# Optimization experiments

Hardware: AMD Instinct MI355X
Metric: run time of the kernel (lower is better)

The kernel has to match this reference:

```python
import jax, jax.numpy as jnp
import numpy as np

HIDDEN = 2048
NUM_Q_HEADS = 32
NUM_KV_HEADS = 8
HEAD_DIM = HIDDEN // NUM_Q_HEADS  # 64
GROUPS = NUM_Q_HEADS // NUM_KV_HEADS  # 4
MAX_WAVELENGTH = 10000.0
B, S = 2, 1024
NEG_INF = -1e9  # keras Softmax masking constant


def apply_rope(x, start_index=0, max_wavelength=MAX_WAVELENGTH):
    # x: [b, s, h, d]; keras_hub RotaryEmbedding (split-half / Llama style)
    d = x.shape[-1]
    s = x.shape[1]
    freq_range = jnp.arange(0, d, 2, dtype=jnp.float32)
    inverse_freq = 1.0 / (max_wavelength ** (freq_range / d))  # [d/2]
    positions = jnp.arange(s, dtype=jnp.float32) + start_index
    freq = positions[:, None] * inverse_freq[None, :]  # [s, d/2]
    emb = jnp.concatenate([freq, freq], axis=-1)[None, :, None, :]  # [1,s,1,d]
    cos = jnp.cos(emb).astype(x.dtype)
    sin = jnp.sin(emb).astype(x.dtype)
    x1, x2 = jnp.split(x, 2, axis=-1)
    half_rot = jnp.concatenate([-x2, x1], axis=-1)
    return x * cos + half_rot * sin


def setup_inputs() -> dict:
    key = jax.random.key(0)
    k1, k2, k3, k4, k5 = jax.random.split(key, 5)
    hidden_states = jax.random.normal(k1, (B, S, HIDDEN), dtype=jnp.float32)
    # causal mask, broadcast over batch
    attention_mask = jnp.broadcast_to(
        jnp.tril(jnp.ones((S, S), dtype=bool))[None], (B, S, S)
    )
    scale = 1.0 / np.sqrt(HIDDEN)
    Wq = jax.random.normal(k2, (HIDDEN, NUM_Q_HEADS * HEAD_DIM), dtype=jnp.float32) * scale
    Wk = jax.random.normal(k3, (HIDDEN, NUM_KV_HEADS * HEAD_DIM), dtype=jnp.float32) * scale
    Wv = jax.random.normal(k4, (HIDDEN, NUM_KV_HEADS * HEAD_DIM), dtype=jnp.float32) * scale
    Wo = jax.random.normal(k5, (NUM_Q_HEADS * HEAD_DIM, HIDDEN), dtype=jnp.float32) * scale
    return {"hidden_states": hidden_states, "attention_mask": attention_mask,
            "Wq": Wq, "Wk": Wk, "Wv": Wv, "Wo": Wo}


def reference(hidden_states, attention_mask, Wq, Wk, Wv, Wo):
    b, s, _ = hidden_states.shape
    q = (hidden_states @ Wq).reshape(b, s, NUM_Q_HEADS, HEAD_DIM)
    k = (hidden_states @ Wk).reshape(b, s, NUM_KV_HEADS, HEAD_DIM)
    v = (hidden_states @ Wv).reshape(b, s, NUM_KV_HEADS, HEAD_DIM)
    q = apply_rope(q)
    k = apply_rope(k)
    # GQA: repeat kv heads to match query heads (ops.repeat on axis 2)
    k = jnp.repeat(k, GROUPS, axis=2)
    v = jnp.repeat(v, GROUPS, axis=2)
    inv_norm = 1.0 / np.sqrt(HEAD_DIM)
    scores = jnp.einsum("bquh,bkuh->buqk", q, k) * inv_norm  # [b, h, q, k]
    scores = scores.astype(jnp.float32)
    scores = jnp.where(attention_mask[:, None, :, :], scores, NEG_INF)
    probs = jax.nn.softmax(scores, axis=-1).astype(hidden_states.dtype)
    attn = jnp.einsum("buqk,bkuh->bquh", probs, v)  # [b, q, h, hd]
    attn = attn.reshape(b, s, HIDDEN)
    return attn @ Wo
```

## Files before the change

kernel.cpp:

```cpp
#include <hip/hip_runtime.h>
#include <hip/hip_bf16.h>
#include <math.h>

#define S_LEN 1024
#define BATCH 2
#define HIDDEN 2048
#define NQH 32
#define NKVH 8
#define HD 64
#define LDQKV 3072
#define M_ROWS (BATCH * S_LEN)

typedef __attribute__((ext_vector_type(8))) short bf16x8;
typedef __attribute__((ext_vector_type(4))) float f32x4;

typedef unsigned int uint32_g __attribute__((address_space(1)));
typedef unsigned int uint32_l __attribute__((address_space(3)));

static __device__ __forceinline__ void load_lds16(const void* g, void* l) {
    __builtin_amdgcn_global_load_lds((const uint32_g*)g, (uint32_l*)l, 16, 0, 0);
}

static __device__ __forceinline__ short f2bf(float f) {
    union { __hip_bfloat16 h; short s; } cv;
    cv.h = __float2bfloat16(f);
    return cv.s;
}

__global__ __launch_bounds__(256) void conv_all_kernel(
    const float* __restrict__ X,
    const float* __restrict__ Wq, const float* __restrict__ Wk,
    const float* __restrict__ Wv, const float* __restrict__ Wo,
    short* __restrict__ Xb, short* __restrict__ Wqkvt, short* __restrict__ Wot,
    float2* __restrict__ cs2)
{
    __shared__ short Ts[64][68];
    const int tid = threadIdx.x;

    if (blockIdx.z == 4) {
        int flat = blockIdx.y * 32 + blockIdx.x;
        size_t base = (size_t)flat * 4096 + (size_t)tid * 16;
        #pragma unroll
        for (int rep = 0; rep < 2; ++rep) {
            size_t i = base + rep * 8;
            float4 a = *reinterpret_cast<const float4*>(X + i);
            float4 b = *reinterpret_cast<const float4*>(X + i + 4);
            union { bf16x8 v; short s[8]; } t;
            t.s[0] = f2bf(a.x); t.s[1] = f2bf(a.y); t.s[2] = f2bf(a.z); t.s[3] = f2bf(a.w);
            t.s[4] = f2bf(b.x); t.s[5] = f2bf(b.y); t.s[6] = f2bf(b.z); t.s[7] = f2bf(b.w);
            *reinterpret_cast<bf16x8*>(Xb + i) = t.v;
        }
        if (flat < 128) {
            int g = flat * 256 + tid;
            int s = g >> 5, i = g & 31;
            float inv_freq = 1.0f / powf(10000.0f, (float)i / 32.0f);
            float freq = (float)s * inv_freq;
            double sn, cs;
            sincos((double)freq, &sn, &cs);
            cs2[g] = make_float2((float)cs, (float)sn);
        }
        return;
    }

    const float* src; short* dst; int N;
    switch (blockIdx.z) {
        case 0: src = Wq; dst = Wqkvt;                         N = 2048; break;
        case 1: src = Wk; dst = Wqkvt + (size_t)2048 * 2048;   N = 512;  break;
        case 2: src = Wv; dst = Wqkvt + (size_t)2560 * 2048;   N = 512;  break;
        default: src = Wo; dst = Wot;                          N = 2048; break;
    }
    const int n0 = blockIdx.x * 64, k0 = blockIdx.y * 64;
    if (n0 >= N) return;

    #pragma unroll
    for (int rep = 0; rep < 4; ++rep) {
        int idx = rep * 256 + tid;
        int row = idx >> 4, c4 = (idx & 15) * 4;
        float4 v = *reinterpret_cast<const float4*>(
            src + (size_t)(k0 + row) * N + n0 + c4);
        ushort4 u;
        u.x = (unsigned short)f2bf(v.x); u.y = (unsigned short)f2bf(v.y);
        u.z = (unsigned short)f2bf(v.z); u.w = (unsigned short)f2bf(v.w);
        *reinterpret_cast<ushort4*>(&Ts[row][c4]) = u;
    }
    __syncthreads();
    #pragma unroll
    for (int rep = 0; rep < 2; ++rep) {
        int idx = rep * 256 + tid;
        int n = idx >> 3, kc = (idx & 7) * 8;
        union { bf16x8 v; short s[8]; } t;
        #pragma unroll
        for (int j = 0; j < 8; ++j) t.s[j] = Ts[kc + j][n];
        *reinterpret_cast<bf16x8*>(dst + (size_t)(n0 + n) * 2048 + k0 + kc) = t.v;
    }
}

template <bool ROPE_BF16>
__global__ __launch_bounds__(256) void gemm_bf16_kernel(
    const short* __restrict__ A, const short* __restrict__ Bt,
    float* __restrict__ C, short* __restrict__ Cb,
    const float2* __restrict__ cs2, int K, int ldc)
{
    const int n0 = blockIdx.x * 128, m0 = blockIdx.y * 128;
    const int tid = threadIdx.x;
    const int w = tid >> 6, lane = tid & 63;
    const int wm = w & 1, wn = w >> 1;
    const int m15 = lane & 15, q4 = lane >> 4;

    __shared__ short As[128][64];
    __shared__ short Bs[128][64];

    f32x4 acc[4][4];
    #pragma unroll
    for (int i = 0; i < 4; ++i)
        #pragma unroll
        for (int j = 0; j < 4; ++j) acc[i][j] = (f32x4){0.f, 0.f, 0.f, 0.f};

    const int srow = lane >> 3;
    const int pchunk = lane & 7;

    for (int k0 = 0; k0 < K; k0 += 64) {
        __syncthreads();
        #pragma unroll
        for (int r = 0; r < 4; ++r) {
            int row = (w * 4 + r) * 8 + srow;
            int lchunk = pchunk ^ (row & 7);
            load_lds16(A + (size_t)(m0 + row) * K + k0 + lchunk * 8,
                       &As[(w * 4 + r) * 8][0]);
            load_lds16(Bt + (size_t)(n0 + row) * K + k0 + lchunk * 8,
                       &Bs[(w * 4 + r) * 8][0]);
        }
        __syncthreads();

        #pragma unroll
        for (int ch = 0; ch < 2; ++ch) {
            bf16x8 af[4], bf[4];
            #pragma unroll
            for (int mt = 0; mt < 4; ++mt) {
                int row = wm * 64 + mt * 16 + m15;
                af[mt] = *reinterpret_cast<const bf16x8*>(
                    &As[row][(((ch * 4 + q4) ^ (row & 7))) * 8]);
            }
            #pragma unroll
            for (int nt = 0; nt < 4; ++nt) {
                int row = wn * 64 + nt * 16 + m15;
                bf[nt] = *reinterpret_cast<const bf16x8*>(
                    &Bs[row][(((ch * 4 + q4) ^ (row & 7))) * 8]);
            }
            #pragma unroll
            for (int mt = 0; mt < 4; ++mt)
                #pragma unroll
                for (int nt = 0; nt < 4; ++nt)
                    acc[mt][nt] = __builtin_amdgcn_mfma_f32_16x16x32_bf16(
                        af[mt], bf[nt], acc[mt][nt], 0, 0, 0);
        }
    }

    const int colbase = n0 + wn * 64;
    if (!ROPE_BF16) {
        #pragma unroll
        for (int mt = 0; mt < 4; ++mt)
            #pragma unroll
            for (int nt = 0; nt < 4; ++nt)
                #pragma unroll
                for (int reg = 0; reg < 4; ++reg)
                    C[(size_t)(m0 + wm * 64 + mt * 16 + q4 * 4 + reg) * ldc
                      + colbase + nt * 16 + m15] = acc[mt][nt][reg];
    } else if (colbase >= 2560) {
        #pragma unroll
        for (int mt = 0; mt < 4; ++mt)
            #pragma unroll
            for (int nt = 0; nt < 4; ++nt)
                #pragma unroll
                for (int reg = 0; reg < 4; ++reg)
                    Cb[(size_t)(m0 + wm * 64 + mt * 16 + q4 * 4 + reg) * ldc
                       + colbase + nt * 16 + m15] = f2bf(acc[mt][nt][reg]);
    } else {
        #pragma unroll
        for (int mt = 0; mt < 4; ++mt) {
            #pragma unroll
            for (int reg = 0; reg < 4; ++reg) {
                int row = m0 + wm * 64 + mt * 16 + q4 * 4 + reg;
                int s = row & (S_LEN - 1);
                float2 t0 = cs2[s * 32 + m15];
                float2 t1 = cs2[s * 32 + 16 + m15];
                float a0 = acc[mt][0][reg], a1 = acc[mt][1][reg];
                float a2 = acc[mt][2][reg], a3 = acc[mt][3][reg];
                size_t base = (size_t)row * ldc + colbase + m15;
                Cb[base +  0] = f2bf(a0 * t0.x - a2 * t0.y);
                Cb[base + 16] = f2bf(a1 * t1.x - a3 * t1.y);
                Cb[base + 32] = f2bf(a2 * t0.x + a0 * t0.y);
                Cb[base + 48] = f2bf(a3 * t1.x + a1 * t1.y);
            }
        }
    }
}

__global__ __launch_bounds__(256) void vtrans_kernel(
    const short* __restrict__ qkvb, short* __restrict__ vt_g)
{
    __shared__ short Ts[128][72];
    const int k0 = blockIdx.x * 128;
    const int bk = blockIdx.y;
    const int b = bk >> 3, kvh = bk & 7;
    const int tid = threadIdx.x;

    #pragma unroll
    for (int rep = 0; rep < 4; ++rep) {
        int idx = rep * 256 + tid;
        int key = idx >> 3, c8 = (idx & 7) * 8;
        *reinterpret_cast<bf16x8*>(&Ts[key][c8]) =
            *reinterpret_cast<const bf16x8*>(
                qkvb + (size_t)(b * S_LEN + k0 + key) * LDQKV + 2560 + kvh * 64 + c8);
    }
    __syncthreads();
    #pragma unroll
    for (int rep = 0; rep < 4; ++rep) {
        int idx = rep * 256 + tid;
        int dim = idx >> 4, kc = (idx & 15) * 8;
        union { bf16x8 v; short s[8]; } t;
        #pragma unroll
        for (int j = 0; j < 8; ++j) t.s[j] = Ts[kc + j][dim];
        *reinterpret_cast<bf16x8*>(
            vt_g + (size_t)(bk * 64 + dim) * S_LEN + k0 + kc) = t.v;
    }
}

__global__ __launch_bounds__(512) void attn_kernel(
    const short* __restrict__ qkvb, const short* __restrict__ vt_g,
    short* __restrict__ attn_b)
{
    const int qt = 7 - blockIdx.x;
    const int h  = blockIdx.y;
    const int b  = blockIdx.z;
    const int tid = threadIdx.x;
    const int w = tid >> 6, lane = tid & 63;
    const int kvh = h >> 2;
    const int m15 = lane & 15, q4 = lane >> 4;

    __shared__ short Ks[64][72];
    __shared__ short Vt[64][72];
    __shared__ float Ps[8][16][68];

    const int rowbase = qt * 128 + w * 16;
    const bf16x8 qf0 = *reinterpret_cast<const bf16x8*>(
        qkvb + (size_t)(b * S_LEN + rowbase + m15) * LDQKV + h * HD + q4 * 8);
    const bf16x8 qf1 = *reinterpret_cast<const bf16x8*>(
        qkvb + (size_t)(b * S_LEN + rowbase + m15) * LDQKV + h * HD + 32 + q4 * 8);

    f32x4 o4[4];
    #pragma unroll
    for (int i = 0; i < 4; ++i) o4[i] = (f32x4){0.f, 0.f, 0.f, 0.f};
    float lsum[4] = {0.f, 0.f, 0.f, 0.f};

    const int ntiles = qt * 2 + 2;
    const int j8 = tid >> 3, c8 = (tid & 7) * 8;
    const short* kbase = qkvb + (size_t)(b * S_LEN) * LDQKV + 2048 + kvh * HD;
    const short* vbase = vt_g + (size_t)((b * 8 + kvh) * 64 + j8) * S_LEN;

    for (int t = 0; t < ntiles; ++t) {
        __syncthreads();
        *reinterpret_cast<bf16x8*>(&Ks[j8][c8]) =
            *reinterpret_cast<const bf16x8*>(kbase + (size_t)(t * 64 + j8) * LDQKV + c8);
        *reinterpret_cast<bf16x8*>(&Vt[j8][c8]) =
            *reinterpret_cast<const bf16x8*>(vbase + t * 64 + c8);
        __syncthreads();

        #pragma unroll
        for (int nt = 0; nt < 4; ++nt) {
            f32x4 acc = (f32x4){0.f, 0.f, 0.f, 0.f};
            bf16x8 kf0 = *reinterpret_cast<const bf16x8*>(&Ks[nt * 16 + m15][q4 * 8]);
            bf16x8 kf1 = *reinterpret_cast<const bf16x8*>(&Ks[nt * 16 + m15][32 + q4 * 8]);
            acc = __builtin_amdgcn_mfma_f32_16x16x32_bf16(qf0, kf0, acc, 0, 0, 0);
            acc = __builtin_amdgcn_mfma_f32_16x16x32_bf16(qf1, kf1, acc, 0, 0, 0);
            int colg = t * 64 + nt * 16 + m15;
            #pragma unroll
            for (int reg = 0; reg < 4; ++reg) {
                int rowg = rowbase + q4 * 4 + reg;
                float sc = acc[reg] * 0.125f;
                float p = (colg <= rowg) ? __expf(fminf(sc, 60.f)) : 0.f;
                lsum[reg] += p;
                Ps[w][q4 * 4 + reg][nt * 16 + m15] = p;
            }
        }

        bf16x8 pf[2];
        #pragma unroll
        for (int ch = 0; ch < 2; ++ch) {
            f32x4 pa = *reinterpret_cast<const f32x4*>(&Ps[w][m15][ch * 32 + q4 * 8]);
            f32x4 pb = *reinterpret_cast<const f32x4*>(&Ps[w][m15][ch * 32 + q4 * 8 + 4]);
            union { bf16x8 v; short s[8]; } tb;
            tb.s[0] = f2bf(pa[0]); tb.s[1] = f2bf(pa[1]);
            tb.s[2] = f2bf(pa[2]); tb.s[3] = f2bf(pa[3]);
            tb.s[4] = f2bf(pb[0]); tb.s[5] = f2bf(pb[1]);
            tb.s[6] = f2bf(pb[2]); tb.s[7] = f2bf(pb[3]);
            pf[ch] = tb.v;
        }

        #pragma unroll
        for (int nt2 = 0; nt2 < 4; ++nt2) {
            bf16x8 vf0 = *reinterpret_cast<const bf16x8*>(&Vt[nt2 * 16 + m15][q4 * 8]);
            bf16x8 vf1 = *reinterpret_cast<const bf16x8*>(&Vt[nt2 * 16 + m15][32 + q4 * 8]);
            o4[nt2] = __builtin_amdgcn_mfma_f32_16x16x32_bf16(pf[0], vf0, o4[nt2], 0, 0, 0);
            o4[nt2] = __builtin_amdgcn_mfma_f32_16x16x32_bf16(pf[1], vf1, o4[nt2], 0, 0, 0);
        }
    }

    float invl[4];
    #pragma unroll
    for (int reg = 0; reg < 4; ++reg) {
        float l = lsum[reg];
        l += __shfl_xor(l, 1, 64);
        l += __shfl_xor(l, 2, 64);
        l += __shfl_xor(l, 4, 64);
        l += __shfl_xor(l, 8, 64);
        invl[reg] = 1.0f / l;
    }

    #pragma unroll
    for (int nt2 = 0; nt2 < 4; ++nt2)
        #pragma unroll
        for (int reg = 0; reg < 4; ++reg)
            attn_b[(size_t)(b * S_LEN + rowbase + q4 * 4 + reg) * HIDDEN
                   + h * HD + nt2 * 16 + m15] = f2bf(o4[nt2][reg] * invl[reg]);
}

extern "C" void kernel_launch(void* const* d_in, const int* in_sizes, int n_in,
                              void* d_out, int out_size, void* d_ws, size_t ws_size,
                              hipStream_t stream) {
    const float* X  = (const float*)d_in[0];
    const float* Wq = (const float*)d_in[2];
    const float* Wk = (const float*)d_in[3];
    const float* Wv = (const float*)d_in[4];
    const float* Wo = (const float*)d_in[5];
    float* out = (float*)d_out;

    short*  qkvb  = (short*)d_ws;
    short*  Xb    = qkvb + (size_t)M_ROWS * LDQKV;
    short*  Wqkvt = Xb + (size_t)HIDDEN * HIDDEN;
    short*  Wot   = Wqkvt + (size_t)LDQKV * HIDDEN;
    short*  vt_g  = Wot + (size_t)HIDDEN * HIDDEN;
    float2* cs2   = (float2*)(vt_g + (size_t)16 * 64 * S_LEN);
    short*  attn_b = Xb;

    conv_all_kernel<<<dim3(32, 32, 5), dim3(256), 0, stream>>>(
        X, Wq, Wk, Wv, Wo, Xb, Wqkvt, Wot, cs2);

    gemm_bf16_kernel<true><<<dim3(24, 16), dim3(256), 0, stream>>>(
        Xb, Wqkvt, nullptr, qkvb, cs2, 2048, LDQKV);
    vtrans_kernel<<<dim3(8, 16), dim3(256), 0, stream>>>(qkvb, vt_g);
    attn_kernel<<<dim3(8, 32, 2), dim3(512), 0, stream>>>(qkvb, vt_g, attn_b);
    gemm_bf16_kernel<false><<<dim3(16, 16), dim3(256), 0, stream>>>(
        attn_b, Wot, out, nullptr, nullptr, 2048, HIDDEN);
}
```

Measured before the change: 231.9 us.

## Shrink GEMM tiles to 128x64 and fuse V transpose into QKV GEMM epilogue

The GEMM tile shrinks from 128x128 to 128x64, doubling the grid (768 and 512 blocks) so more of the CUs are busy. The standalone V-transpose kernel is removed. Blocks covering V columns now transpose their bf16 tile through LDS and write vt_g directly, saving one launch and a round trip through global memory. In exchange, each tile gets less reuse of A per K step, and V blocks no longer write V into qkvb (attention reads only vt_g).

```diff
diff --git a/kernel.cpp b/kernel.cpp
--- a/kernel.cpp
+++ b/kernel.cpp
@@ -99,20 +99,21 @@
 __global__ __launch_bounds__(256) void gemm_bf16_kernel(
     const short* __restrict__ A, const short* __restrict__ Bt,
     float* __restrict__ C, short* __restrict__ Cb,
+    short* __restrict__ vt_g,
     const float2* __restrict__ cs2, int K, int ldc)
 {
-    const int n0 = blockIdx.x * 128, m0 = blockIdx.y * 128;
+    const int n0 = blockIdx.x * 64, m0 = blockIdx.y * 128;
     const int tid = threadIdx.x;
     const int w = tid >> 6, lane = tid & 63;
-    const int wm = w & 1, wn = w >> 1;
     const int m15 = lane & 15, q4 = lane >> 4;
 
-    __shared__ short As[128][64];
-    __shared__ short Bs[128][64];
-
-    f32x4 acc[4][4];
-    #pragma unroll
-    for (int i = 0; i < 4; ++i)
+    __shared__ short SL[128 * 64 + 64 * 64];
+    short (*As)[64] = (short(*)[64])SL;
+    short (*Bs)[64] = (short(*)[64])(SL + 128 * 64);
+
+    f32x4 acc[2][4];
+    #pragma unroll
+    for (int i = 0; i < 2; ++i)
         #pragma unroll
         for (int j = 0; j < 4; ++j) acc[i][j] = (f32x4){0.f, 0.f, 0.f, 0.f};
 
@@ -127,28 +128,33 @@
             int lchunk = pchunk ^ (row & 7);
             load_lds16(A + (size_t)(m0 + row) * K + k0 + lchunk * 8,
                        &As[(w * 4 + r) * 8][0]);
+        }
+        #pragma unroll
+        for (int r = 0; r < 2; ++r) {
+            int row = (w * 2 + r) * 8 + srow;
+            int lchunk = pchunk ^ (row & 7);
             load_lds16(Bt + (size_t)(n0 + row) * K + k0 + lchunk * 8,
-                       &Bs[(w * 4 + r) * 8][0]);
+                       &Bs[(w * 2 + r) * 8][0]);
         }
         __syncthreads();
 
         #pragma unroll
         for (int ch = 0; ch < 2; ++ch) {
-            bf16x8 af[4], bf[4];
-            #pragma unroll
-            for (int mt = 0; mt < 4; ++mt) {
-                int row = wm * 64 + mt * 16 + m15;
+            bf16x8 af[2], bf[4];
+            #pragma unroll
+            for (int mt = 0; mt < 2; ++mt) {
+                int row = w * 32 + mt * 16 + m15;
                 af[mt] = *reinterpret_cast<const bf16x8*>(
                     &As[row][(((ch * 4 + q4) ^ (row & 7))) * 8]);
             }
             #pragma unroll
             for (int nt = 0; nt < 4; ++nt) {
-                int row = wn * 64 + nt * 16 + m15;
+                int row = nt * 16 + m15;
                 bf[nt] = *reinterpret_cast<const bf16x8*>(
                     &Bs[row][(((ch * 4 + q4) ^ (row & 7))) * 8]);
             }
             #pragma unroll
-            for (int mt = 0; mt < 4; ++mt)
+            for (int mt = 0; mt < 2; ++mt)
                 #pragma unroll
                 for (int nt = 0; nt < 4; ++nt)
                     acc[mt][nt] = __builtin_amdgcn_mfma_f32_16x16x32_bf16(
@@ -156,73 +162,58 @@
         }
     }
 
-    const int colbase = n0 + wn * 64;
     if (!ROPE_BF16) {
         #pragma unroll
-        for (int mt = 0; mt < 4; ++mt)
+        for (int mt = 0; mt < 2; ++mt)
             #pragma unroll
             for (int nt = 0; nt < 4; ++nt)
                 #pragma unroll
                 for (int reg = 0; reg < 4; ++reg)
-                    C[(size_t)(m0 + wm * 64 + mt * 16 + q4 * 4 + reg) * ldc
-                      + colbase + nt * 16 + m15] = acc[mt][nt][reg];
-    } else if (colbase >= 2560) {
-        #pragma unroll
-        for (int mt = 0; mt < 4; ++mt)
-            #pragma unroll
-            for (int nt = 0; nt < 4; ++nt)
-                #pragma unroll
-                for (int reg = 0; reg < 4; ++reg)
-                    Cb[(size_t)(m0 + wm * 64 + mt * 16 + q4 * 4 + reg) * ldc
-                       + colbase + nt * 16 + m15] = f2bf(acc[mt][nt][reg]);
-    } else {
-        #pragma unroll
-        for (int mt = 0; mt < 4; ++mt) {
+                    C[(size_t)(m0 + w * 32 + mt * 16 + q4 * 4 + reg) * ldc
+                      + n0 + nt * 16 + m15] = acc[mt][nt][reg];
+    } else if (n0 < 2560) {
+        #pragma unroll
+        for (int mt = 0; mt < 2; ++mt) {
             #pragma unroll
             for (int reg = 0; reg < 4; ++reg) {
-                int row = m0 + wm * 64 + mt * 16 + q4 * 4 + reg;
+                int row = m0 + w * 32 + mt * 16 + q4 * 4 + reg;
                 int s = row & (S_LEN - 1);
                 float2 t0 = cs2[s * 32 + m15];
                 float2 t1 = cs2[s * 32 + 16 + m15];
                 float a0 = acc[mt][0][reg], a1 = acc[mt][1][reg];
                 float a2 = acc[mt][2][reg], a3 = acc[mt][3][reg];
-                size_t base = (size_t)row * ldc + colbase + m15;
+                size_t base = (size_t)row * ldc + n0 + m15;
                 Cb[base +  0] = f2bf(a0 * t0.x - a2 * t0.y);
                 Cb[base + 16] = f2bf(a1 * t1.x - a3 * t1.y);
                 Cb[base + 32] = f2bf(a2 * t0.x + a0 * t0.y);
                 Cb[base + 48] = f2bf(a3 * t1.x + a1 * t1.y);
             }
         }
-    }
-}
-
-__global__ __launch_bounds__(256) void vtrans_kernel(
-    const short* __restrict__ qkvb, short* __restrict__ vt_g)
-{
-    __shared__ short Ts[128][72];
-    const int k0 = blockIdx.x * 128;
-    const int bk = blockIdx.y;
-    const int b = bk >> 3, kvh = bk & 7;
-    const int tid = threadIdx.x;
-
-    #pragma unroll
-    for (int rep = 0; rep < 4; ++rep) {
-        int idx = rep * 256 + tid;
-        int key = idx >> 3, c8 = (idx & 7) * 8;
-        *reinterpret_cast<bf16x8*>(&Ts[key][c8]) =
-            *reinterpret_cast<const bf16x8*>(
-                qkvb + (size_t)(b * S_LEN + k0 + key) * LDQKV + 2560 + kvh * 64 + c8);
-    }
-    __syncthreads();
-    #pragma unroll
-    for (int rep = 0; rep < 4; ++rep) {
-        int idx = rep * 256 + tid;
-        int dim = idx >> 4, kc = (idx & 15) * 8;
-        union { bf16x8 v; short s[8]; } t;
-        #pragma unroll
-        for (int j = 0; j < 8; ++j) t.s[j] = Ts[kc + j][dim];
-        *reinterpret_cast<bf16x8*>(
-            vt_g + (size_t)(bk * 64 + dim) * S_LEN + k0 + kc) = t.v;
+    } else {
+        __syncthreads();
+        short (*VT)[136] = (short(*)[136])SL;
+        #pragma unroll
+        for (int mt = 0; mt < 2; ++mt) {
+            #pragma unroll
+            for (int nt = 0; nt < 4; ++nt) {
+                ushort4 u;
+                u.x = (unsigned short)f2bf(acc[mt][nt][0]);
+                u.y = (unsigned short)f2bf(acc[mt][nt][1]);
+                u.z = (unsigned short)f2bf(acc[mt][nt][2]);
+                u.w = (unsigned short)f2bf(acc[mt][nt][3]);
+                *reinterpret_cast<ushort4*>(
+                    &VT[nt * 16 + m15][w * 32 + mt * 16 + q4 * 4]) = u;
+            }
+        }
+        __syncthreads();
+        const int kvh = (n0 - 2560) >> 6;
+        const int b = m0 >> 10, k0loc = m0 & (S_LEN - 1);
+        const int dim = tid >> 2, kc = (tid & 3) * 32;
+        short* dst = vt_g + (size_t)((b * 8 + kvh) * 64 + dim) * S_LEN + k0loc + kc;
+        #pragma unroll
+        for (int u = 0; u < 4; ++u)
+            *reinterpret_cast<bf16x8*>(dst + u * 8) =
+                *reinterpret_cast<const bf16x8*>(&VT[dim][kc + u * 8]);
     }
 }
 
@@ -346,10 +337,9 @@
     conv_all_kernel<<<dim3(32, 32, 5), dim3(256), 0, stream>>>(
         X, Wq, Wk, Wv, Wo, Xb, Wqkvt, Wot, cs2);
 
-    gemm_bf16_kernel<true><<<dim3(24, 16), dim3(256), 0, stream>>>(
-        Xb, Wqkvt, nullptr, qkvb, cs2, 2048, LDQKV);
-    vtrans_kernel<<<dim3(8, 16), dim3(256), 0, stream>>>(qkvb, vt_g);
+    gemm_bf16_kernel<true><<<dim3(48, 16), dim3(256), 0, stream>>>(
+        Xb, Wqkvt, nullptr, qkvb, vt_g, cs2, 2048, LDQKV);
     attn_kernel<<<dim3(8, 32, 2), dim3(512), 0, stream>>>(qkvb, vt_g, attn_b);
-    gemm_bf16_kernel<false><<<dim3(16, 16), dim3(256), 0, stream>>>(
-        attn_b, Wot, out, nullptr, nullptr, 2048, HIDDEN);
-}
+    gemm_bf16_kernel<false><<<dim3(32, 16), dim3(256), 0, stream>>>(
+        attn_b, Wot, out, nullptr, nullptr, nullptr, 2048, HIDDEN);
+}
```

Measured after the change: 212.3 us. -8.5%, faster.
